# Performance work log

Measured on AMD Instinct MI355X. Metric: run time of the kernel, lower is better.

Reference implementation:

```python
import jax, jax.numpy as jnp
import numpy as np

NUM_TAGS = 20000
H_DIM = 256
EPS = 1e-5


def _layernorm(x, g, b):
    mu = x.mean(-1, keepdims=True)
    var = ((x - mu) ** 2).mean(-1, keepdims=True)
    return (x - mu) * jax.lax.rsqrt(var + EPS) * g + b


def setup_inputs() -> dict:
    key = jax.random.key(0)
    ks = jax.random.split(key, 16)
    B, F, T = 64, 128, 16
    h4 = H_DIM * 4
    s = 0.02
    return {
        "tags": jax.random.randint(ks[0], (B, F, T), 0, NUM_TAGS),
        "feature_counts": jax.random.uniform(ks[1], (B,), jnp.float32) * 100.0,
        # tag_norm LayerNorm(num_tags)
        "ln_g": jnp.ones((NUM_TAGS,), jnp.float32),
        "ln_b": jnp.zeros((NUM_TAGS,), jnp.float32),
        # encoder: Linear(num_tags+1 -> 4h), GELU, LayerNorm(4h), MLP(4h->4h->h)
        "w1": jax.random.normal(ks[2], (NUM_TAGS + 1, h4), jnp.float32) * s,
        "b1": jnp.zeros((h4,), jnp.float32),
        "ln2_g": jnp.ones((h4,), jnp.float32),
        "ln2_b": jnp.zeros((h4,), jnp.float32),
        "we1": jax.random.normal(ks[3], (h4, h4), jnp.float32) * s,
        "be1": jnp.zeros((h4,), jnp.float32),
        "we2": jax.random.normal(ks[4], (h4, H_DIM), jnp.float32) * s,
        "be2": jnp.zeros((H_DIM,), jnp.float32),
        # decoder: MLP(h -> 4h -> num_tags+1)
        "wd1": jax.random.normal(ks[5], (H_DIM, h4), jnp.float32) * s,
        "bd1": jnp.zeros((h4,), jnp.float32),
        "wd2": jax.random.normal(ks[6], (h4, NUM_TAGS + 1), jnp.float32) * s,
        "bd2": jnp.zeros((NUM_TAGS + 1,), jnp.float32),
    }


def reference(tags, feature_counts, ln_g, ln_b, w1, b1, ln2_g, ln2_b,
              we1, be1, we2, be2, wd1, bd1, wd2, bd2):
    B, F, T = tags.shape
    # multi_hot.scatter_(2, tags, 1).clamp_(0,1): duplicates within a row collapse to 1
    bi = jnp.arange(B)[:, None, None]
    fi = jnp.arange(F)[None, :, None]
    multi_hot = jnp.zeros((B, F, NUM_TAGS), jnp.float32).at[bi, fi, tags].set(1.0)
    tile_tag_count = multi_hot.sum(axis=1)  # [B, num_tags]

    yn = _layernorm(tile_tag_count, ln_g, ln_b)
    y = jnp.concatenate([feature_counts[:, None] / 100.0, yn], axis=1)  # [B, num_tags+1]

    # encoder
    h = jax.nn.gelu(y @ w1 + b1, approximate=False)
    h = _layernorm(h, ln2_g, ln2_b)
    h = jax.nn.gelu(h @ we1 + be1, approximate=False)
    enc = h @ we2 + be2  # [B, h_dim]

    # decoder
    d = jax.nn.gelu(enc @ wd1 + bd1, approximate=False)
    dec = d @ wd2 + bd2  # [B, num_tags+1]
    return (y, enc, dec)
```

## Files before the change

### kernel.cpp

```cpp
#include <hip/hip_runtime.h>
#include <math.h>

#define NUM_TAGS 20000
#define BATCH 64
#define H4 1024
#define HD 256
#define NT1 20001

__device__ __forceinline__ float gelu_exact(float x) {
    return 0.5f * x * (1.0f + erff(x * 0.7071067811865476f));
}

typedef const __attribute__((address_space(1))) void* gp_t;
typedef __attribute__((address_space(3))) void* lp_t;
__device__ __forceinline__ void async_ld4(const float* g, float* lds_base) {
    __builtin_amdgcn_global_load_lds((gp_t)g, (lp_t)lds_base, 4, 0, 0);
}
__device__ __forceinline__ void async_ld16(const float* g, float* lds_base) {
    __builtin_amdgcn_global_load_lds((gp_t)g, (lp_t)lds_base, 16, 0, 0);
}

__global__ __launch_bounds__(256) void k_scatter(const int* __restrict__ tags,
                                                 int* __restrict__ counts) {
    int g = blockIdx.x * 256 + threadIdx.x;
    int b = g >> 7;
    const int* tp = tags + ((size_t)g << 4);
    int t[16];
#pragma unroll
    for (int i = 0; i < 16; ++i) t[i] = tp[i];
#pragma unroll
    for (int i = 0; i < 16; ++i) {
        bool dup = false;
        for (int j = 0; j < i; ++j) dup = dup || (t[j] == t[i]);
        if (!dup) atomicAdd(&counts[(size_t)b * NUM_TAGS + t[i]], 1);
    }
}

__global__ __launch_bounds__(256) void k_ln1_stats(const int* __restrict__ counts,
                                                   float* __restrict__ stats) {
    int b = blockIdx.y, c = blockIdx.x, tid = threadIdx.x;
    const int* crow = counts + (size_t)b * NUM_TAGS;
    int lo = c * 2500, hi = lo + 2500;
    float s = 0.f, s2 = 0.f;
    for (int t = lo + tid; t < hi; t += 256) {
        float v = (float)crow[t];
        s += v; s2 += v * v;
    }
#pragma unroll
    for (int off = 32; off > 0; off >>= 1) {
        s  += __shfl_down(s, off);
        s2 += __shfl_down(s2, off);
    }
    __shared__ float ls[4], ls2[4];
    int wave = tid >> 6;
    if ((tid & 63) == 0) { ls[wave] = s; ls2[wave] = s2; }
    __syncthreads();
    if (tid == 0) {
        stats[(b * 8 + c) * 2 + 0] = ls[0] + ls[1] + ls[2] + ls[3];
        stats[(b * 8 + c) * 2 + 1] = ls2[0] + ls2[1] + ls2[2] + ls2[3];
    }
}

__global__ __launch_bounds__(256) void k_ln1_apply(const int* __restrict__ counts,
                                                   const float* __restrict__ fc,
                                                   const float* __restrict__ lng,
                                                   const float* __restrict__ lnb,
                                                   const float* __restrict__ stats,
                                                   float* __restrict__ y) {
    int b = blockIdx.y, c = blockIdx.x, tid = threadIdx.x;
    float S = 0.f, S2 = 0.f;
#pragma unroll
    for (int i = 0; i < 8; ++i) {
        S  += stats[(b * 8 + i) * 2 + 0];
        S2 += stats[(b * 8 + i) * 2 + 1];
    }
    float mu = S / (float)NUM_TAGS;
    float var = S2 / (float)NUM_TAGS - mu * mu;
    float rs = rsqrtf(var + 1e-5f);
    const int* crow = counts + (size_t)b * NUM_TAGS;
    float* yrow = y + (size_t)b * NT1;
    if (c == 0 && tid == 0) yrow[0] = fc[b] * 0.01f;
    int lo = c * 2500, hi = lo + 2500;
    for (int t = lo + tid; t < hi; t += 256) {
        float v = (float)crow[t];
        yrow[1 + t] = (v - mu) * rs * lng[t] + lnb[t];
    }
}

template <int PATH>
__global__ __launch_bounds__(256, 2) void k_gemm(const float* __restrict__ A, int lda,
                                                 const float* __restrict__ W, int ldw,
                                                 float* __restrict__ P,
                                                 int N, int kpb) {
    __shared__ __align__(16) float As[4][512];
    __shared__ __align__(16) float Ws[4][2048];
    const int tid = threadIdx.x;
    const int lane = tid & 63, wid = tid >> 6;
    const int tn = tid & 31, tb = tid >> 5;
    const int n0 = blockIdx.x * 256;
    const int kstart = blockIdx.y * kpb;
    const int nchunk = kpb >> 3;

    float acc[8][8];
#pragma unroll
    for (int i = 0; i < 8; ++i)
#pragma unroll
        for (int j = 0; j < 8; ++j) acc[i][j] = 0.f;

    auto issue = [&](int b, int c) {
        int k0 = kstart + c * 8;
#pragma unroll
        for (int j = 0; j < 2; ++j) {
            int d0 = j * 256 + wid * 64;
            int d = d0 + lane;
            async_ld4(A + (size_t)(d >> 3) * lda + k0 + (d & 7), &As[b][d0]);
        }
        if (PATH == 0) {
#pragma unroll
            for (int j = 0; j < 2; ++j) {
                int g0 = j * 256 + wid * 64;
                int g = g0 + lane;
                int kk = g >> 6, c4 = g & 63;
                async_ld16(W + (size_t)(k0 + kk) * ldw + n0 + c4 * 4, &Ws[b][g0 * 4]);
            }
        } else {
#pragma unroll
            for (int j = 0; j < 8; ++j) {
                int d0 = j * 256 + wid * 64;
                int d = d0 + lane;
                int kk = d >> 8, cc = d & 255;
                async_ld4(W + (size_t)(k0 + kk) * ldw + min(n0 + cc, N - 1), &Ws[b][d0]);
            }
        }
    };

    issue(0, 0);
    if (nchunk > 1) issue(1, 1);

    for (int c = 0; c < nchunk; ++c) {
        if (c + 2 < nchunk) issue((c + 2) & 3, c + 2);
        int ahead = nchunk - 1 - c;
        if (PATH == 0) {
            if (ahead >= 2)      asm volatile("s_waitcnt vmcnt(8)"  ::: "memory");
            else if (ahead == 1) asm volatile("s_waitcnt vmcnt(4)"  ::: "memory");
            else                 asm volatile("s_waitcnt vmcnt(0)"  ::: "memory");
        } else {
            if (ahead >= 2)      asm volatile("s_waitcnt vmcnt(20)" ::: "memory");
            else if (ahead == 1) asm volatile("s_waitcnt vmcnt(10)" ::: "memory");
            else                 asm volatile("s_waitcnt vmcnt(0)"  ::: "memory");
        }
        __builtin_amdgcn_s_barrier();
        asm volatile("" ::: "memory");

        const float* Ab = As[c & 3];
        const float* Wb = Ws[c & 3];
        __builtin_amdgcn_s_setprio(1);
#pragma unroll
        for (int k4 = 0; k4 < 2; ++k4) {
            float4 a4[8];
#pragma unroll
            for (int i = 0; i < 8; ++i)
                a4[i] = *(const float4*)&Ab[(tb * 8 + i) * 8 + k4 * 4];
#pragma unroll
            for (int kl = 0; kl < 4; ++kl) {
                const float4 w0 = *(const float4*)&Wb[(k4 * 4 + kl) * 256 + tn * 4];
                const float4 w1 = *(const float4*)&Wb[(k4 * 4 + kl) * 256 + 128 + tn * 4];
                const float wv[8] = {w0.x, w0.y, w0.z, w0.w, w1.x, w1.y, w1.z, w1.w};
#pragma unroll
                for (int i = 0; i < 8; ++i) {
                    float av = (kl == 0) ? a4[i].x : (kl == 1) ? a4[i].y
                             : (kl == 2) ? a4[i].z : a4[i].w;
#pragma unroll
                    for (int jj = 0; jj < 8; ++jj)
                        acc[i][jj] = fmaf(av, wv[jj], acc[i][jj]);
                }
            }
        }
        __builtin_amdgcn_s_setprio(0);
        asm volatile("" ::: "memory");
    }

    float* Pp = P + ((size_t)blockIdx.x * gridDim.y + blockIdx.y) * 16384;
#pragma unroll
    for (int i = 0; i < 8; ++i) {
        int row = tb * 8 + i;
        float4 v0 = {acc[i][0], acc[i][1], acc[i][2], acc[i][3]};
        float4 v1 = {acc[i][4], acc[i][5], acc[i][6], acc[i][7]};
        *(float4*)&Pp[row * 256 + tn * 4]       = v0;
        *(float4*)&Pp[row * 256 + 128 + tn * 4] = v1;
    }
}

template <bool GELU>
__global__ __launch_bounds__(256) void k_reduce(const float* __restrict__ P, int KS,
                                                const float* __restrict__ bias,
                                                const float* __restrict__ r1row,
                                                const float* __restrict__ fc,
                                                float* __restrict__ out, int ldo, int N) {
    int b = blockIdx.y;
    int n = blockIdx.x * 256 + threadIdx.x;
    if (n >= N) return;
    int nb = n >> 8, col = n & 255;
    const float* p = P + (size_t)nb * KS * 16384 + b * 256 + col;
    float s0 = 0.f, s1 = 0.f, s2 = 0.f, s3 = 0.f;
    int k = 0;
    for (; k + 3 < KS; k += 4) {
        s0 += p[(size_t)(k + 0) * 16384];
        s1 += p[(size_t)(k + 1) * 16384];
        s2 += p[(size_t)(k + 2) * 16384];
        s3 += p[(size_t)(k + 3) * 16384];
    }
    for (; k < KS; ++k) s0 += p[(size_t)k * 16384];
    float s = (s0 + s1) + (s2 + s3) + bias[n];
    if (r1row) s += fc[b] * 0.01f * r1row[n];
    if (GELU) s = gelu_exact(s);
    out[(size_t)b * ldo + n] = s;
}

__global__ __launch_bounds__(256) void k_ln2(const float* __restrict__ g1,
                                             const float* __restrict__ lng,
                                             const float* __restrict__ lnb,
                                             float* __restrict__ h2) {
    int b = blockIdx.x, tid = threadIdx.x;
    float v[4];
    float s = 0.f, s2 = 0.f;
#pragma unroll
    for (int j = 0; j < 4; ++j) {
        int nidx = tid + 256 * j;
        float x = g1[b * H4 + nidx];
        v[j] = x;
        s += x; s2 += x * x;
    }
#pragma unroll
    for (int off = 32; off > 0; off >>= 1) {
        s  += __shfl_down(s, off);
        s2 += __shfl_down(s2, off);
    }
    __shared__ float ls[4], ls2[4], smu, srs;
    int wave = tid >> 6;
    if ((tid & 63) == 0) { ls[wave] = s; ls2[wave] = s2; }
    __syncthreads();
    if (tid == 0) {
        float S  = ls[0] + ls[1] + ls[2] + ls[3];
        float S2 = ls2[0] + ls2[1] + ls2[2] + ls2[3];
        float mu = S / (float)H4;
        float var = S2 / (float)H4 - mu * mu;
        smu = mu;
        srs = rsqrtf(var + 1e-5f);
    }
    __syncthreads();
    float mu = smu, rs = srs;
#pragma unroll
    for (int j = 0; j < 4; ++j) {
        int nidx = tid + 256 * j;
        h2[b * H4 + nidx] = (v[j] - mu) * rs * lng[nidx] + lnb[nidx];
    }
}

extern "C" void kernel_launch(void* const* d_in, const int* in_sizes, int n_in,
                              void* d_out, int out_size, void* d_ws, size_t ws_size,
                              hipStream_t stream) {
    (void)in_sizes; (void)n_in; (void)out_size;
    const int*   tags  = (const int*)d_in[0];
    const float* fc    = (const float*)d_in[1];
    const float* ln_g  = (const float*)d_in[2];
    const float* ln_b  = (const float*)d_in[3];
    const float* w1    = (const float*)d_in[4];
    const float* b1    = (const float*)d_in[5];
    const float* ln2_g = (const float*)d_in[6];
    const float* ln2_b = (const float*)d_in[7];
    const float* we1   = (const float*)d_in[8];
    const float* be1   = (const float*)d_in[9];
    const float* we2   = (const float*)d_in[10];
    const float* be2   = (const float*)d_in[11];
    const float* wd1   = (const float*)d_in[12];
    const float* bd1   = (const float*)d_in[13];
    const float* wd2   = (const float*)d_in[14];
    const float* bd2   = (const float*)d_in[15];

    float* out = (float*)d_out;
    float* y   = out;
    float* enc = out + (size_t)BATCH * NT1;
    float* dec = enc + BATCH * HD;

    char* ws = (char*)d_ws;
    size_t off = 0;
    int*   counts = (int*)(ws + off);   off += (size_t)BATCH * NUM_TAGS * 4;
    float* stats  = (float*)(ws + off); off += 64 * 8 * 2 * 4;
    float* g1     = (float*)(ws + off); off += (size_t)BATCH * H4 * 4;
    float* h2     = (float*)(ws + off); off += (size_t)BATCH * H4 * 4;
    float* g2     = (float*)(ws + off); off += (size_t)BATCH * H4 * 4;
    float* dd     = (float*)(ws + off); off += (size_t)BATCH * H4 * 4;
    float* arena  = (float*)(ws + off);
    size_t avail  = (ws_size > off) ? (ws_size - off) : 0;

    const size_t MB = 1024 * 1024;
    int KS1, KS5;
    if (avail >= 45 * MB)      { KS1 = 125; KS5 = 8; }
    else if (avail >= 33 * MB) { KS1 = 125; KS5 = 4; }
    else if (avail >= 17 * MB) { KS1 = 63;  KS5 = 4; }
    else                       { KS1 = 63;  KS5 = 2; }
    int kpb5 = H4 / KS5;
    (void)KS1;

    hipMemsetAsync(counts, 0, (size_t)BATCH * NUM_TAGS * 4, stream);
    k_scatter<<<32, 256, 0, stream>>>(tags, counts);
    k_ln1_stats<<<dim3(8, 64), 256, 0, stream>>>(counts, stats);
    k_ln1_apply<<<dim3(8, 64), 256, 0, stream>>>(counts, fc, ln_g, ln_b, stats, y);

    k_gemm<0><<<dim3(4, 125), 256, 0, stream>>>(y + 1, NT1, w1 + H4, H4, arena, H4, 160);
    k_reduce<true><<<dim3(4, 64), 256, 0, stream>>>(arena, 125, b1, w1, fc, g1, H4, H4);
    k_ln2<<<64, 256, 0, stream>>>(g1, ln2_g, ln2_b, h2);

    k_gemm<0><<<dim3(4, 32), 256, 0, stream>>>(h2, H4, we1, H4, arena, H4, 32);
    k_reduce<true><<<dim3(4, 64), 256, 0, stream>>>(arena, 32, be1, nullptr, nullptr, g2, H4, H4);

    k_gemm<0><<<dim3(1, 32), 256, 0, stream>>>(g2, H4, we2, HD, arena, HD, 32);
    k_reduce<false><<<dim3(1, 64), 256, 0, stream>>>(arena, 32, be2, nullptr, nullptr, enc, HD, HD);

    k_gemm<0><<<dim3(4, 16), 256, 0, stream>>>(enc, HD, wd1, H4, arena, H4, 16);
    k_reduce<true><<<dim3(4, 64), 256, 0, stream>>>(arena, 16, bd1, nullptr, nullptr, dd, H4, H4);

    k_gemm<1><<<dim3(79, KS5), 256, 0, stream>>>(dd, H4, wd2, NT1, arena, NT1, kpb5);
    k_reduce<false><<<dim3(79, 64), 256, 0, stream>>>(arena, KS5, bd2, nullptr, nullptr, dec, NT1, NT1);
}
```

Measured before the change: 330.9 us.

## Restructure GEMM to 512 threads with direct A loads and double buffering

The split-K GEMM moves to 512-thread blocks where each wave owns 8 batch rows and each lane owns 4 output columns, giving 8x4 accumulators per thread instead of 8x8. The A tile is no longer staged in LDS; threads read A straight from global memory as wave-uniform loads. The W pipeline shrinks from 4-deep to a double buffer synchronised with __syncthreads. The final decoder reduction is vectorised to float4 and the scatter launch is reshaped. The trade is less register pressure and more waves against less work per thread and more global traffic for A, plus a shallower prefetch.

New measurement: 344.5 us. 1.04x slower.

```diff
diff --git a/kernel.cpp b/kernel.cpp
--- a/kernel.cpp
+++ b/kernel.cpp
@@ -11,6 +11,8 @@
     return 0.5f * x * (1.0f + erff(x * 0.7071067811865476f));
 }
 
+struct F4 { float x, y, z, w; };
+
 typedef const __attribute__((address_space(1))) void* gp_t;
 typedef __attribute__((address_space(3))) void* lp_t;
 __device__ __forceinline__ void async_ld4(const float* g, float* lds_base) {
@@ -20,9 +22,9 @@
     __builtin_amdgcn_global_load_lds((gp_t)g, (lp_t)lds_base, 16, 0, 0);
 }
 
-__global__ __launch_bounds__(256) void k_scatter(const int* __restrict__ tags,
+__global__ __launch_bounds__(128) void k_scatter(const int* __restrict__ tags,
                                                  int* __restrict__ counts) {
-    int g = blockIdx.x * 256 + threadIdx.x;
+    int g = blockIdx.x * 128 + threadIdx.x;
     int b = g >> 7;
     const int* tp = tags + ((size_t)g << 4);
     int t[16];
@@ -88,107 +90,74 @@
 }
 
 template <int PATH>
-__global__ __launch_bounds__(256, 2) void k_gemm(const float* __restrict__ A, int lda,
+__global__ __launch_bounds__(512, 2) void k_gemm(const float* __restrict__ A, int lda,
                                                  const float* __restrict__ W, int ldw,
                                                  float* __restrict__ P,
                                                  int N, int kpb) {
-    __shared__ __align__(16) float As[4][512];
-    __shared__ __align__(16) float Ws[4][2048];
+    __shared__ __align__(16) float Ws[2][2048];
     const int tid = threadIdx.x;
-    const int lane = tid & 63, wid = tid >> 6;
-    const int tn = tid & 31, tb = tid >> 5;
+    const int lane = tid & 63;
+    const int wid = __builtin_amdgcn_readfirstlane(tid >> 6);
+    const int wrow = wid * 8;
     const int n0 = blockIdx.x * 256;
     const int kstart = blockIdx.y * kpb;
     const int nchunk = kpb >> 3;
 
-    float acc[8][8];
-#pragma unroll
-    for (int i = 0; i < 8; ++i)
-#pragma unroll
-        for (int j = 0; j < 8; ++j) acc[i][j] = 0.f;
+    float4 acc[8];
+#pragma unroll
+    for (int i = 0; i < 8; ++i) acc[i] = make_float4(0.f, 0.f, 0.f, 0.f);
 
     auto issue = [&](int b, int c) {
         int k0 = kstart + c * 8;
-#pragma unroll
-        for (int j = 0; j < 2; ++j) {
-            int d0 = j * 256 + wid * 64;
-            int d = d0 + lane;
-            async_ld4(A + (size_t)(d >> 3) * lda + k0 + (d & 7), &As[b][d0]);
-        }
         if (PATH == 0) {
-#pragma unroll
-            for (int j = 0; j < 2; ++j) {
-                int g0 = j * 256 + wid * 64;
-                int g = g0 + lane;
-                int kk = g >> 6, c4 = g & 63;
-                async_ld16(W + (size_t)(k0 + kk) * ldw + n0 + c4 * 4, &Ws[b][g0 * 4]);
-            }
+            int kk = tid >> 6, c4 = tid & 63;
+            async_ld16(W + (size_t)(k0 + kk) * ldw + n0 + c4 * 4, &Ws[b][wid * 256]);
         } else {
 #pragma unroll
-            for (int j = 0; j < 8; ++j) {
-                int d0 = j * 256 + wid * 64;
-                int d = d0 + lane;
+            for (int j = 0; j < 4; ++j) {
+                int d = j * 512 + tid;
                 int kk = d >> 8, cc = d & 255;
-                async_ld4(W + (size_t)(k0 + kk) * ldw + min(n0 + cc, N - 1), &Ws[b][d0]);
+                async_ld4(W + (size_t)(k0 + kk) * ldw + min(n0 + cc, N - 1),
+                          &Ws[b][j * 512 + wid * 64]);
             }
         }
     };
 
     issue(0, 0);
-    if (nchunk > 1) issue(1, 1);
 
     for (int c = 0; c < nchunk; ++c) {
-        if (c + 2 < nchunk) issue((c + 2) & 3, c + 2);
-        int ahead = nchunk - 1 - c;
-        if (PATH == 0) {
-            if (ahead >= 2)      asm volatile("s_waitcnt vmcnt(8)"  ::: "memory");
-            else if (ahead == 1) asm volatile("s_waitcnt vmcnt(4)"  ::: "memory");
-            else                 asm volatile("s_waitcnt vmcnt(0)"  ::: "memory");
-        } else {
-            if (ahead >= 2)      asm volatile("s_waitcnt vmcnt(20)" ::: "memory");
-            else if (ahead == 1) asm volatile("s_waitcnt vmcnt(10)" ::: "memory");
-            else                 asm volatile("s_waitcnt vmcnt(0)"  ::: "memory");
-        }
-        __builtin_amdgcn_s_barrier();
-        asm volatile("" ::: "memory");
-
-        const float* Ab = As[c & 3];
-        const float* Wb = Ws[c & 3];
+        __syncthreads();
+        if (c + 1 < nchunk) issue((c + 1) & 1, c + 1);
+        const float* Wb = Ws[c & 1];
+        const int k0 = kstart + c * 8;
         __builtin_amdgcn_s_setprio(1);
 #pragma unroll
         for (int k4 = 0; k4 < 2; ++k4) {
-            float4 a4[8];
+            F4 a[8];
 #pragma unroll
             for (int i = 0; i < 8; ++i)
-                a4[i] = *(const float4*)&Ab[(tb * 8 + i) * 8 + k4 * 4];
+                a[i] = *(const F4*)(A + (size_t)(wrow + i) * lda + k0 + k4 * 4);
 #pragma unroll
             for (int kl = 0; kl < 4; ++kl) {
-                const float4 w0 = *(const float4*)&Wb[(k4 * 4 + kl) * 256 + tn * 4];
-                const float4 w1 = *(const float4*)&Wb[(k4 * 4 + kl) * 256 + 128 + tn * 4];
-                const float wv[8] = {w0.x, w0.y, w0.z, w0.w, w1.x, w1.y, w1.z, w1.w};
+                const float4 w = *(const float4*)&Wb[(k4 * 4 + kl) * 256 + lane * 4];
 #pragma unroll
                 for (int i = 0; i < 8; ++i) {
-                    float av = (kl == 0) ? a4[i].x : (kl == 1) ? a4[i].y
-                             : (kl == 2) ? a4[i].z : a4[i].w;
-#pragma unroll
-                    for (int jj = 0; jj < 8; ++jj)
-                        acc[i][jj] = fmaf(av, wv[jj], acc[i][jj]);
+                    float av = (kl == 0) ? a[i].x : (kl == 1) ? a[i].y
+                             : (kl == 2) ? a[i].z : a[i].w;
+                    acc[i].x = fmaf(av, w.x, acc[i].x);
+                    acc[i].y = fmaf(av, w.y, acc[i].y);
+                    acc[i].z = fmaf(av, w.z, acc[i].z);
+                    acc[i].w = fmaf(av, w.w, acc[i].w);
                 }
             }
         }
         __builtin_amdgcn_s_setprio(0);
-        asm volatile("" ::: "memory");
     }
 
     float* Pp = P + ((size_t)blockIdx.x * gridDim.y + blockIdx.y) * 16384;
 #pragma unroll
-    for (int i = 0; i < 8; ++i) {
-        int row = tb * 8 + i;
-        float4 v0 = {acc[i][0], acc[i][1], acc[i][2], acc[i][3]};
-        float4 v1 = {acc[i][4], acc[i][5], acc[i][6], acc[i][7]};
-        *(float4*)&Pp[row * 256 + tn * 4]       = v0;
-        *(float4*)&Pp[row * 256 + 128 + tn * 4] = v1;
-    }
+    for (int i = 0; i < 8; ++i)
+        *(float4*)&Pp[(wrow + i) * 256 + lane * 4] = acc[i];
 }
 
 template <bool GELU>
@@ -215,6 +184,32 @@
     if (r1row) s += fc[b] * 0.01f * r1row[n];
     if (GELU) s = gelu_exact(s);
     out[(size_t)b * ldo + n] = s;
+}
+
+__global__ __launch_bounds__(256) void k_reduce_v4(const float* __restrict__ P, int KS,
+                                                   const float* __restrict__ bias,
+                                                   float* __restrict__ out, int ldo, int N) {
+    int b = blockIdx.y;
+    int n = (blockIdx.x * 256 + threadIdx.x) * 4;
+    if (n >= N) return;
+    int nb = n >> 8, col = n & 255;
+    const float* p = P + (size_t)nb * KS * 16384 + b * 256 + col;
+    if (n + 3 < N) {
+        float sx = 0.f, sy = 0.f, sz = 0.f, sw = 0.f;
+        for (int k = 0; k < KS; ++k) {
+            float4 v = *(const float4*)&p[(size_t)k * 16384];
+            sx += v.x; sy += v.y; sz += v.z; sw += v.w;
+        }
+        F4 bi = *(const F4*)&bias[n];
+        F4 r = {sx + bi.x, sy + bi.y, sz + bi.z, sw + bi.w};
+        *(F4*)&out[(size_t)b * ldo + n] = r;
+    } else {
+        for (int j = 0; n + j < N; ++j) {
+            float s = 0.f;
+            for (int k = 0; k < KS; ++k) s += p[(size_t)k * 16384 + j];
+            out[(size_t)b * ldo + n + j] = s + bias[n + j];
+        }
+    }
 }
 
 __global__ __launch_bounds__(256) void k_ln2(const float* __restrict__ g1,
@@ -304,23 +299,23 @@
     (void)KS1;
 
     hipMemsetAsync(counts, 0, (size_t)BATCH * NUM_TAGS * 4, stream);
-    k_scatter<<<32, 256, 0, stream>>>(tags, counts);
+    k_scatter<<<64, 128, 0, stream>>>(tags, counts);
     k_ln1_stats<<<dim3(8, 64), 256, 0, stream>>>(counts, stats);
     k_ln1_apply<<<dim3(8, 64), 256, 0, stream>>>(counts, fc, ln_g, ln_b, stats, y);
 
-    k_gemm<0><<<dim3(4, 125), 256, 0, stream>>>(y + 1, NT1, w1 + H4, H4, arena, H4, 160);
+    k_gemm<0><<<dim3(4, 125), 512, 0, stream>>>(y + 1, NT1, w1 + H4, H4, arena, H4, 160);
     k_reduce<true><<<dim3(4, 64), 256, 0, stream>>>(arena, 125, b1, w1, fc, g1, H4, H4);
     k_ln2<<<64, 256, 0, stream>>>(g1, ln2_g, ln2_b, h2);
 
-    k_gemm<0><<<dim3(4, 32), 256, 0, stream>>>(h2, H4, we1, H4, arena, H4, 32);
+    k_gemm<0><<<dim3(4, 32), 512, 0, stream>>>(h2, H4, we1, H4, arena, H4, 32);
     k_reduce<true><<<dim3(4, 64), 256, 0, stream>>>(arena, 32, be1, nullptr, nullptr, g2, H4, H4);
 
-    k_gemm<0><<<dim3(1, 32), 256, 0, stream>>>(g2, H4, we2, HD, arena, HD, 32);
+    k_gemm<0><<<dim3(1, 32), 512, 0, stream>>>(g2, H4, we2, HD, arena, HD, 32);
     k_reduce<false><<<dim3(1, 64), 256, 0, stream>>>(arena, 32, be2, nullptr, nullptr, enc, HD, HD);
 
-    k_gemm<0><<<dim3(4, 16), 256, 0, stream>>>(enc, HD, wd1, H4, arena, H4, 16);
+    k_gemm<0><<<dim3(4, 16), 512, 0, stream>>>(enc, HD, wd1, H4, arena, H4, 16);
     k_reduce<true><<<dim3(4, 64), 256, 0, stream>>>(arena, 16, bd1, nullptr, nullptr, dd, H4, H4);
 
-    k_gemm<1><<<dim3(79, KS5), 256, 0, stream>>>(dd, H4, wd2, NT1, arena, NT1, kpb5);
-    k_reduce<false><<<dim3(79, 64), 256, 0, stream>>>(arena, KS5, bd2, nullptr, nullptr, dec, NT1, NT1);
-}
+    k_gemm<1><<<dim3(79, KS5), 512, 0, stream>>>(dd, H4, wd2, NT1, arena, NT1, kpb5);
+    k_reduce_v4<<<dim3(20, 64), 256, 0, stream>>>(arena, KS5, bd2, dec, NT1, NT1);
+}
```

## Fuse tag histogram and first layernorm into one LDS kernel; vectorize final reduce

Applied to the files above, without the earlier changes.

Replaces the memset, global-atomic scatter, stats kernel and apply kernel with one kernel per batch row. It builds the tag histogram in an 80KB LDS array and computes the layernorm in place. This removes the 5MB global counts buffer and three launches, at the cost of only 64 blocks with a large LDS footprint. The final decoder split-K reduction now uses float4 loads with a scalar tail.

Measured after the change: 320.1 us. 3.3% less time.

```diff
diff --git a/kernel.cpp b/kernel.cpp
--- a/kernel.cpp
+++ b/kernel.cpp
@@ -11,6 +11,8 @@
     return 0.5f * x * (1.0f + erff(x * 0.7071067811865476f));
 }
 
+struct F4 { float x, y, z, w; };
+
 typedef const __attribute__((address_space(1))) void* gp_t;
 typedef __attribute__((address_space(3))) void* lp_t;
 __device__ __forceinline__ void async_ld4(const float* g, float* lds_base) {
@@ -20,30 +22,35 @@
     __builtin_amdgcn_global_load_lds((gp_t)g, (lp_t)lds_base, 16, 0, 0);
 }
 
-__global__ __launch_bounds__(256) void k_scatter(const int* __restrict__ tags,
-                                                 int* __restrict__ counts) {
-    int g = blockIdx.x * 256 + threadIdx.x;
-    int b = g >> 7;
-    const int* tp = tags + ((size_t)g << 4);
-    int t[16];
-#pragma unroll
-    for (int i = 0; i < 16; ++i) t[i] = tp[i];
-#pragma unroll
-    for (int i = 0; i < 16; ++i) {
-        bool dup = false;
-        for (int j = 0; j < i; ++j) dup = dup || (t[j] == t[i]);
-        if (!dup) atomicAdd(&counts[(size_t)b * NUM_TAGS + t[i]], 1);
-    }
-}
-
-__global__ __launch_bounds__(256) void k_ln1_stats(const int* __restrict__ counts,
-                                                   float* __restrict__ stats) {
-    int b = blockIdx.y, c = blockIdx.x, tid = threadIdx.x;
-    const int* crow = counts + (size_t)b * NUM_TAGS;
-    int lo = c * 2500, hi = lo + 2500;
+__global__ __launch_bounds__(1024) void k_ln1_fused(const int* __restrict__ tags,
+                                                    const float* __restrict__ fc,
+                                                    const float* __restrict__ lng,
+                                                    const float* __restrict__ lnb,
+                                                    float* __restrict__ y) {
+    __shared__ int hist[NUM_TAGS];
+    __shared__ float ls[16], ls2[16], smu, srs;
+    const int b = blockIdx.x, tid = threadIdx.x;
+
+    for (int t = tid; t < NUM_TAGS; t += 1024) hist[t] = 0;
+    __syncthreads();
+
+    if (tid < 128) {
+        const int* tp = tags + ((size_t)(b * 128 + tid) << 4);
+        int t[16];
+#pragma unroll
+        for (int i = 0; i < 16; ++i) t[i] = tp[i];
+#pragma unroll
+        for (int i = 0; i < 16; ++i) {
+            bool dup = false;
+            for (int j = 0; j < i; ++j) dup = dup || (t[j] == t[i]);
+            if (!dup) atomicAdd(&hist[t[i]], 1);
+        }
+    }
+    __syncthreads();
+
     float s = 0.f, s2 = 0.f;
-    for (int t = lo + tid; t < hi; t += 256) {
-        float v = (float)crow[t];
+    for (int t = tid; t < NUM_TAGS; t += 1024) {
+        float v = (float)hist[t];
         s += v; s2 += v * v;
     }
 #pragma unroll
@@ -51,38 +58,25 @@
         s  += __shfl_down(s, off);
         s2 += __shfl_down(s2, off);
     }
-    __shared__ float ls[4], ls2[4];
     int wave = tid >> 6;
     if ((tid & 63) == 0) { ls[wave] = s; ls2[wave] = s2; }
     __syncthreads();
     if (tid == 0) {
-        stats[(b * 8 + c) * 2 + 0] = ls[0] + ls[1] + ls[2] + ls[3];
-        stats[(b * 8 + c) * 2 + 1] = ls2[0] + ls2[1] + ls2[2] + ls2[3];
-    }
-}
-
-__global__ __launch_bounds__(256) void k_ln1_apply(const int* __restrict__ counts,
-                                                   const float* __restrict__ fc,
-                                                   const float* __restrict__ lng,
-                                                   const float* __restrict__ lnb,
-                                                   const float* __restrict__ stats,
-                                                   float* __restrict__ y) {
-    int b = blockIdx.y, c = blockIdx.x, tid = threadIdx.x;
-    float S = 0.f, S2 = 0.f;
-#pragma unroll
-    for (int i = 0; i < 8; ++i) {
-        S  += stats[(b * 8 + i) * 2 + 0];
-        S2 += stats[(b * 8 + i) * 2 + 1];
-    }
-    float mu = S / (float)NUM_TAGS;
-    float var = S2 / (float)NUM_TAGS - mu * mu;
-    float rs = rsqrtf(var + 1e-5f);
-    const int* crow = counts + (size_t)b * NUM_TAGS;
+        float S = 0.f, S2 = 0.f;
+#pragma unroll
+        for (int i = 0; i < 16; ++i) { S += ls[i]; S2 += ls2[i]; }
+        float mu = S / (float)NUM_TAGS;
+        float var = S2 / (float)NUM_TAGS - mu * mu;
+        smu = mu;
+        srs = rsqrtf(var + 1e-5f);
+    }
+    __syncthreads();
+    float mu = smu, rs = srs;
+
     float* yrow = y + (size_t)b * NT1;
-    if (c == 0 && tid == 0) yrow[0] = fc[b] * 0.01f;
-    int lo = c * 2500, hi = lo + 2500;
-    for (int t = lo + tid; t < hi; t += 256) {
-        float v = (float)crow[t];
+    if (tid == 0) yrow[0] = fc[b] * 0.01f;
+    for (int t = tid; t < NUM_TAGS; t += 1024) {
+        float v = (float)hist[t];
         yrow[1 + t] = (v - mu) * rs * lng[t] + lnb[t];
     }
 }
@@ -215,6 +209,32 @@
     if (r1row) s += fc[b] * 0.01f * r1row[n];
     if (GELU) s = gelu_exact(s);
     out[(size_t)b * ldo + n] = s;
+}
+
+__global__ __launch_bounds__(256) void k_reduce_v4(const float* __restrict__ P, int KS,
+                                                   const float* __restrict__ bias,
+                                                   float* __restrict__ out, int ldo, int N) {
+    int b = blockIdx.y;
+    int n = (blockIdx.x * 256 + threadIdx.x) * 4;
+    if (n >= N) return;
+    int nb = n >> 8, col = n & 255;
+    const float* p = P + (size_t)nb * KS * 16384 + b * 256 + col;
+    if (n + 3 < N) {
+        float sx = 0.f, sy = 0.f, sz = 0.f, sw = 0.f;
+        for (int k = 0; k < KS; ++k) {
+            float4 v = *(const float4*)&p[(size_t)k * 16384];
+            sx += v.x; sy += v.y; sz += v.z; sw += v.w;
+        }
+        F4 bi = *(const F4*)&bias[n];
+        F4 r = {sx + bi.x, sy + bi.y, sz + bi.z, sw + bi.w};
+        *(F4*)&out[(size_t)b * ldo + n] = r;
+    } else {
+        for (int j = 0; n + j < N; ++j) {
+            float s = 0.f;
+            for (int k = 0; k < KS; ++k) s += p[(size_t)k * 16384 + j];
+            out[(size_t)b * ldo + n + j] = s + bias[n + j];
+        }
+    }
 }
 
 __global__ __launch_bounds__(256) void k_ln2(const float* __restrict__ g1,
@@ -285,8 +305,6 @@
 
     char* ws = (char*)d_ws;
     size_t off = 0;
-    int*   counts = (int*)(ws + off);   off += (size_t)BATCH * NUM_TAGS * 4;
-    float* stats  = (float*)(ws + off); off += 64 * 8 * 2 * 4;
     float* g1     = (float*)(ws + off); off += (size_t)BATCH * H4 * 4;
     float* h2     = (float*)(ws + off); off += (size_t)BATCH * H4 * 4;
     float* g2     = (float*)(ws + off); off += (size_t)BATCH * H4 * 4;
@@ -295,18 +313,14 @@
     size_t avail  = (ws_size > off) ? (ws_size - off) : 0;
 
     const size_t MB = 1024 * 1024;
-    int KS1, KS5;
-    if (avail >= 45 * MB)      { KS1 = 125; KS5 = 8; }
-    else if (avail >= 33 * MB) { KS1 = 125; KS5 = 4; }
-    else if (avail >= 17 * MB) { KS1 = 63;  KS5 = 4; }
-    else                       { KS1 = 63;  KS5 = 2; }
+    int KS5;
+    if (avail >= 45 * MB)      { KS5 = 8; }
+    else if (avail >= 33 * MB) { KS5 = 4; }
+    else if (avail >= 17 * MB) { KS5 = 4; }
+    else                       { KS5 = 2; }
     int kpb5 = H4 / KS5;
-    (void)KS1;
-
-    hipMemsetAsync(counts, 0, (size_t)BATCH * NUM_TAGS * 4, stream);
-    k_scatter<<<32, 256, 0, stream>>>(tags, counts);
-    k_ln1_stats<<<dim3(8, 64), 256, 0, stream>>>(counts, stats);
-    k_ln1_apply<<<dim3(8, 64), 256, 0, stream>>>(counts, fc, ln_g, ln_b, stats, y);
+
+    k_ln1_fused<<<64, 1024, 0, stream>>>(tags, fc, ln_g, ln_b, y);
 
     k_gemm<0><<<dim3(4, 125), 256, 0, stream>>>(y + 1, NT1, w1 + H4, H4, arena, H4, 160);
     k_reduce<true><<<dim3(4, 64), 256, 0, stream>>>(arena, 125, b1, w1, fc, g1, H4, H4);
@@ -322,5 +336,5 @@
     k_reduce<true><<<dim3(4, 64), 256, 0, stream>>>(arena, 16, bd1, nullptr, nullptr, dd, H4, H4);
 
     k_gemm<1><<<dim3(79, KS5), 256, 0, stream>>>(dd, H4, wd2, NT1, arena, NT1, kpb5);
-    k_reduce<false><<<dim3(79, 64), 256, 0, stream>>>(arena, KS5, bd2, nullptr, nullptr, dec, NT1, NT1);
-}
+    k_reduce_v4<<<dim3(20, 64), 256, 0, stream>>>(arena, KS5, bd2, dec, NT1, NT1);
+}
```
